# Performance work log

Measured on AMD Instinct MI355X. Metric: run time of the kernel, lower is better.

## Reference

```python
import jax, jax.numpy as jnp
import numpy as np

B, IN, OUT, NVAL = 8192, 4096, 4096, 1024

def setup_inputs() -> dict:
    key = jax.random.key(0)
    k1, k2, k3 = jax.random.split(key, 3)
    x = jax.random.normal(k1, (B, IN), dtype=jnp.float32)
    values = jnp.sort(jax.random.normal(k2, (NVAL,), dtype=jnp.float32))
    bias = jnp.zeros((OUT,), dtype=jnp.float32)
    w_idx = jax.random.randint(k3, (OUT, IN), 0, NVAL, dtype=jnp.int64)
    return {"x": x, "values": values, "bias": bias, "w_idx": w_idx}

def reference(x, values, bias, w_idx):
    # Gather dense weight [OUT, IN] from the codebook, then F.linear: x @ W^T + b
    weight = values[w_idx]
    return jnp.einsum('bi,oi->bo', x, weight) + bias
```

## Files before the change

### kernel.cpp

```cpp
#include <hip/hip_runtime.h>
#include <cstdint>
#include <cstddef>


#define BB 8192
#define KK 4096
#define OO 4096
#define NVALS 1024
#define BM 256
#define BN 256
#define BKT 64

typedef unsigned short u16;
typedef __bf16 bf16x8 __attribute__((ext_vector_type(8)));
typedef float f32x4 __attribute__((ext_vector_type(4)));
typedef unsigned short u16x8 __attribute__((ext_vector_type(8)));
typedef int i32x4 __attribute__((ext_vector_type(4)));

__device__ __forceinline__ u16 f2bf(float f) {
  uint32_t u = __builtin_bit_cast(uint32_t, f);
  u += 0x7FFFu + ((u >> 16) & 1u);
  return (u16)(u >> 16);
}

__global__ void cast_x_kernel(const float* __restrict__ x, u16* __restrict__ xh,
                              int n8) {
  int stride = gridDim.x * blockDim.x;
  for (int i = blockIdx.x * blockDim.x + threadIdx.x; i < n8; i += stride) {
    f32x4 v0 = ((const f32x4*)x)[2 * i];
    f32x4 v1 = ((const f32x4*)x)[2 * i + 1];
    u16x8 h;
#pragma unroll
    for (int j = 0; j < 4; ++j) {
      h[j] = f2bf(v0[j]);
      h[4 + j] = f2bf(v1[j]);
    }
    ((u16x8*)xh)[i] = h;
  }
}

__global__ void dequant_w_kernel(const int* __restrict__ w_idx,
                                 const float* __restrict__ values,
                                 u16* __restrict__ wh, int n8) {
  __shared__ u16 vtab[NVALS];
  for (int i = threadIdx.x; i < NVALS; i += blockDim.x) vtab[i] = f2bf(values[i]);
  __syncthreads();
  int stride = gridDim.x * blockDim.x;
  for (int i = blockIdx.x * blockDim.x + threadIdx.x; i < n8; i += stride) {
    i32x4 a = ((const i32x4*)w_idx)[2 * i];
    i32x4 b = ((const i32x4*)w_idx)[2 * i + 1];
    u16x8 h;
#pragma unroll
    for (int j = 0; j < 4; ++j) {
      h[j] = vtab[a[j] & (NVALS - 1)];
      h[4 + j] = vtab[b[j] & (NVALS - 1)];
    }
    ((u16x8*)wh)[i] = h;
  }
}

__device__ __forceinline__ void stage16(const u16* g, u16* l) {
  __builtin_amdgcn_global_load_lds(
      (const __attribute__((address_space(1))) uint32_t*)g,
      (__attribute__((address_space(3))) uint32_t*)l, 16, 0, 0);
}
__device__ __forceinline__ bf16x8 ldfrag(const u16* p) {
  return __builtin_bit_cast(bf16x8, *(const u16x8*)p);
}
#define BAR()                               \
  do {                                      \
    __asm__ volatile("" ::: "memory");      \
    __builtin_amdgcn_s_barrier();           \
    __asm__ volatile("" ::: "memory");      \
  } while (0)
#define VMCNT6() __asm__ volatile("s_waitcnt vmcnt(6)" ::: "memory")
#define VMCNT0() __asm__ volatile("s_waitcnt vmcnt(0)" ::: "memory")

template <int MH, int NH>
__device__ __forceinline__ void mfma_quad(bf16x8 (&aR)[4][2], bf16x8 (&bR)[4][2],
                                          f32x4 (&acc)[8][4]) {
  __builtin_amdgcn_s_setprio(1);
#pragma unroll
  for (int mq = 0; mq < 4; ++mq)
#pragma unroll
    for (int n2 = 0; n2 < 2; ++n2)
#pragma unroll
      for (int kk = 0; kk < 2; ++kk)
        acc[MH * 4 + mq][NH * 2 + n2] = __builtin_amdgcn_mfma_f32_16x16x32_bf16(
            aR[mq][kk], bR[NH * 2 + n2][kk], acc[MH * 4 + mq][NH * 2 + n2], 0, 0, 0);
  __builtin_amdgcn_s_setprio(0);
}

template <bool ST1, bool ST2, int VM>
__device__ __forceinline__ void ktile(
    u16* CA, u16* CB, u16* OA, const u16* __restrict__ xh,
    const u16* __restrict__ wh, size_t kY, size_t k2, size_t (&srcAX)[2],
    size_t (&srcBX)[2], int (&dstAX)[2], int (&dstBX)[2], int adr, int bdr,
    int chk0, int chk1, bf16x8 (&aR)[4][2], bf16x8 (&bR)[4][2],
    f32x4 (&acc)[8][4]) {
  constexpr size_t srcAY = (size_t)64 * KK;
  constexpr size_t srcBY = (size_t)32 * KK;
  constexpr int dstAY = 64 * BKT;
  constexpr int dstBY = 32 * BKT;
#pragma unroll
  for (int mq = 0; mq < 4; ++mq) {
    aR[mq][0] = ldfrag(CA + adr + chk0 + mq * 1024);
    aR[mq][1] = ldfrag(CA + adr + chk1 + mq * 1024);
  }
#pragma unroll
  for (int n = 0; n < 2; ++n) {
    bR[n][0] = ldfrag(CB + bdr + chk0 + n * 1024);
    bR[n][1] = ldfrag(CB + bdr + chk1 + n * 1024);
  }
  if (ST1) {
#pragma unroll
    for (int i = 0; i < 2; ++i)
      stage16(xh + srcAX[i] + srcAY + kY, OA + dstAX[i] + dstAY);
  }
  BAR();
  mfma_quad<0, 0>(aR, bR, acc);
  BAR();
#pragma unroll
  for (int n = 2; n < 4; ++n) {
    bR[n][0] = ldfrag(CB + bdr + chk0 + n * 1024);
    bR[n][1] = ldfrag(CB + bdr + chk1 + n * 1024);
  }
  if (ST2) {
#pragma unroll
    for (int i = 0; i < 2; ++i) stage16(xh + srcAX[i] + k2, CA + dstAX[i]);
  }
  BAR();
  mfma_quad<0, 1>(aR, bR, acc);
  BAR();
#pragma unroll
  for (int mq = 0; mq < 4; ++mq) {
    aR[mq][0] = ldfrag(CA + adr + chk0 + (4 + mq) * 1024);
    aR[mq][1] = ldfrag(CA + adr + chk1 + (4 + mq) * 1024);
  }
  if (ST2) {
#pragma unroll
    for (int i = 0; i < 2; ++i) stage16(wh + srcBX[i] + k2, CB + dstBX[i]);
  }
  BAR();
  mfma_quad<1, 1>(aR, bR, acc);
  BAR();
  if (ST2) {
#pragma unroll
    for (int i = 0; i < 2; ++i)
      stage16(wh + srcBX[i] + srcBY + k2, CB + dstBX[i] + dstBY);
  }
  BAR();
  mfma_quad<1, 0>(aR, bR, acc);
  if (VM == 0) VMCNT6();
  if (VM == 1) VMCNT0();
  BAR();
}

__global__ __launch_bounds__(512, 2) void gemm8_kernel(
    const u16* __restrict__ xh, const u16* __restrict__ wh,
    const float* __restrict__ bias, float* __restrict__ out) {
  __shared__ __align__(16) u16 lds[4 * BM * BKT];
  u16* const A0 = lds;
  u16* const A1 = lds + BM * BKT;
  u16* const B0 = lds + 2 * BM * BKT;
  u16* const B1 = lds + 3 * BM * BKT;

  int wg = blockIdx.x;
  int cpx = gridDim.x >> 3;
  int swz = (wg & 7) * cpx + (wg >> 3);
  constexpr int NTN = OO / BN;
  int tm = swz / NTN;
  int tn = swz % NTN;

  const int t = threadIdx.x;
  const int lane = t & 63;
  const int wv = t >> 6;
  const int wm = wv >> 2;
  const int wn = wv & 3;

  size_t srcAX[2], srcBX[2];
  int dstAX[2], dstBX[2];
#pragma unroll
  for (int i = 0; i < 2; ++i) {
    int j = i * 512 + t;
    int rl = j >> 3;
    int ch = j & 7;
    int chs = ch ^ (rl & 7);
    int rA = (rl & 63) + ((rl >> 6) << 7);
    int rB = (rl & 31) + ((rl >> 5) << 6);
    srcAX[i] = (size_t)(tm * BM + rA) * KK + chs * 8;
    srcBX[i] = (size_t)(tn * BN + rB) * KK + chs * 8;
    dstAX[i] = rA * BKT + ch * 8;
    dstBX[i] = rB * BKT + ch * 8;
  }
  constexpr size_t srcAY = (size_t)64 * KK;
  constexpr size_t srcBY = (size_t)32 * KK;
  constexpr int dstAY = 64 * BKT;
  constexpr int dstBY = 32 * BKT;

  const int adr = (wm * 128 + (lane & 15)) * BKT;
  const int bdr = (wn * 64 + (lane & 15)) * BKT;
  const int chk0 = (((lane >> 4) ^ (lane & 7))) * 8;
  const int chk1 = ((4 + (lane >> 4)) ^ (lane & 7)) * 8;

  f32x4 acc[8][4];
#pragma unroll
  for (int m = 0; m < 8; ++m)
#pragma unroll
    for (int n = 0; n < 4; ++n) acc[m][n] = f32x4{0.f, 0.f, 0.f, 0.f};
  bf16x8 aR[4][2], bR[4][2];

#pragma unroll
  for (int i = 0; i < 2; ++i) stage16(xh + srcAX[i], A0 + dstAX[i]);
#pragma unroll
  for (int i = 0; i < 2; ++i) stage16(xh + srcAX[i] + srcAY, A0 + dstAX[i] + dstAY);
#pragma unroll
  for (int i = 0; i < 2; ++i) stage16(wh + srcBX[i], B0 + dstBX[i]);
#pragma unroll
  for (int i = 0; i < 2; ++i) stage16(wh + srcBX[i] + srcBY, B0 + dstBX[i] + dstBY);
#pragma unroll
  for (int i = 0; i < 2; ++i) stage16(xh + srcAX[i] + BKT, A1 + dstAX[i]);
#pragma unroll
  for (int i = 0; i < 2; ++i) stage16(wh + srcBX[i] + BKT, B1 + dstBX[i]);
#pragma unroll
  for (int i = 0; i < 2; ++i)
    stage16(wh + srcBX[i] + srcBY + BKT, B1 + dstBX[i] + dstBY);
  VMCNT6();
  BAR();

#pragma unroll 1
  for (int it = 0; it < 31; ++it) {
    size_t s0 = 2 * (size_t)it;
    ktile<true, true, 0>(A0, B0, A1, xh, wh, (s0 + 1) * BKT, (s0 + 2) * BKT,
                         srcAX, srcBX, dstAX, dstBX, adr, bdr, chk0, chk1, aR,
                         bR, acc);
    ktile<true, true, 0>(A1, B1, A0, xh, wh, (s0 + 2) * BKT, (s0 + 3) * BKT,
                         srcAX, srcBX, dstAX, dstBX, adr, bdr, chk0, chk1, aR,
                         bR, acc);
  }
  ktile<true, false, 1>(A0, B0, A1, xh, wh, (size_t)63 * BKT, 0, srcAX, srcBX,
                        dstAX, dstBX, adr, bdr, chk0, chk1, aR, bR, acc);
  ktile<false, false, 2>(A1, B1, A0, xh, wh, 0, 0, srcAX, srcBX, dstAX, dstBX,
                         adr, bdr, chk0, chk1, aR, bR, acc);

#pragma unroll
  for (int n = 0; n < 4; ++n) {
    int col = tn * BN + wn * 64 + n * 16 + (lane & 15);
    float bv = bias[col];
#pragma unroll
    for (int m = 0; m < 8; ++m) {
      int row = tm * BM + wm * 128 + m * 16 + ((lane >> 4) << 2);
#pragma unroll
      for (int r = 0; r < 4; ++r)
        out[(size_t)(row + r) * OO + col] = acc[m][n][r] + bv;
    }
  }
}

__global__ __launch_bounds__(256) void gemm_direct_kernel(
    const float* __restrict__ x, const int* __restrict__ w_idx,
    const float* __restrict__ values, const float* __restrict__ bias,
    float* __restrict__ out) {
  constexpr int K = KK;
  constexpr int NTN = OO / 128;
  __shared__ __align__(16) u16 Ah[128 * 32];
  __shared__ __align__(16) u16 Bh[128 * 32];
  __shared__ u16 vtab[NVALS];
  int wg = blockIdx.x;
  int cpx = gridDim.x >> 3;
  int swz = (wg & 7) * cpx + (wg >> 3);
  int tm = swz / NTN, tn = swz % NTN;
  int t = threadIdx.x, lane = t & 63, wave = t >> 6;
  int wr = wave >> 1, wc = wave & 1;
  for (int i = t; i < NVALS; i += 256) vtab[i] = f2bf(values[i]);
  __syncthreads();
  int r0 = t >> 2, cb = (t & 3) * 8;
  const size_t arow = (size_t)(tm * 128 + r0) * K + cb;
  const size_t brow = (size_t)(tn * 128 + r0) * K + cb;
  const size_t half_off = (size_t)64 * K;
  const int dst = t * 8;
  f32x4 acc[4][4];
#pragma unroll
  for (int m = 0; m < 4; ++m)
#pragma unroll
    for (int n = 0; n < 4; ++n) acc[m][n] = f32x4{0.f, 0.f, 0.f, 0.f};
  const int a_off = (wr * 64 + (lane & 15)) * 32 + (lane >> 4) * 8;
  const int b_off = (wc * 64 + (lane & 15)) * 32 + (lane >> 4) * 8;
  for (int kt = 0; kt < K; kt += 32) {
#pragma unroll
    for (int hh = 0; hh < 2; ++hh) {
      const float* s = x + arow + (size_t)hh * half_off + kt;
      f32x4 v0 = *(const f32x4*)s;
      f32x4 v1 = *(const f32x4*)(s + 4);
      u16x8 hv;
#pragma unroll
      for (int j = 0; j < 4; ++j) {
        hv[j] = f2bf(v0[j]);
        hv[4 + j] = f2bf(v1[j]);
      }
      *(u16x8*)(Ah + dst + hh * 2048) = hv;
    }
#pragma unroll
    for (int hh = 0; hh < 2; ++hh) {
      const int* s = w_idx + brow + (size_t)hh * half_off + kt;
      i32x4 i0v = *(const i32x4*)s;
      i32x4 i1v = *(const i32x4*)(s + 4);
      u16x8 hv;
#pragma unroll
      for (int j = 0; j < 4; ++j) {
        hv[j] = vtab[i0v[j] & (NVALS - 1)];
        hv[4 + j] = vtab[i1v[j] & (NVALS - 1)];
      }
      *(u16x8*)(Bh + dst + hh * 2048) = hv;
    }
    __syncthreads();
    bf16x8 ahf[4], bhf[4];
#pragma unroll
    for (int m = 0; m < 4; ++m) ahf[m] = ldfrag(Ah + a_off + m * 512);
#pragma unroll
    for (int n = 0; n < 4; ++n) bhf[n] = ldfrag(Bh + b_off + n * 512);
#pragma unroll
    for (int m = 0; m < 4; ++m)
#pragma unroll
      for (int n = 0; n < 4; ++n)
        acc[m][n] = __builtin_amdgcn_mfma_f32_16x16x32_bf16(ahf[m], bhf[n],
                                                            acc[m][n], 0, 0, 0);
    __syncthreads();
  }
  float bv[4];
  int coln[4];
#pragma unroll
  for (int n = 0; n < 4; ++n) {
    coln[n] = tn * 128 + wc * 64 + n * 16 + (lane & 15);
    bv[n] = bias[coln[n]];
  }
#pragma unroll
  for (int m = 0; m < 4; ++m) {
    int rowb = tm * 128 + wr * 64 + m * 16 + (lane >> 4) * 4;
#pragma unroll
    for (int n = 0; n < 4; ++n)
#pragma unroll
      for (int r = 0; r < 4; ++r)
        out[(size_t)(rowb + r) * OO + coln[n]] = acc[m][n][r] + bv[n];
  }
}

extern "C" void kernel_launch(void* const* d_in, const int* in_sizes, int n_in,
                              void* d_out, int out_size, void* d_ws, size_t ws_size,
                              hipStream_t stream) {
  const float* x      = (const float*)d_in[0];
  const float* values = (const float*)d_in[1];
  const float* bias   = (const float*)d_in[2];
  const int*   w_idx  = (const int*)d_in[3];
  float* out = (float*)d_out;

  const size_t xN = (size_t)BB * KK;
  const size_t wN = (size_t)OO * KK;
  const size_t need = (xN + wN) * sizeof(u16);

  if (ws_size >= need) {
    u16* xh = (u16*)d_ws;
    u16* wh = xh + xN;
    cast_x_kernel<<<2048, 256, 0, stream>>>(x, xh, (int)(xN / 8));
    dequant_w_kernel<<<2048, 256, 0, stream>>>(w_idx, values, wh, (int)(wN / 8));
    dim3 grid((BB / BM) * (OO / BN));
    gemm8_kernel<<<grid, 512, 0, stream>>>(xh, wh, bias, out);
  } else {
    dim3 grid((BB / 128) * (OO / 128));
    gemm_direct_kernel<<<grid, 256, 0, stream>>>(x, w_idx, values, bias, out);
  }
}
```

Before: 487.0 us.

## Reorder MFMA phases by K-half and rebalance async LDS staging across phases

Splits each k-tile's MFMA work by k-half (KI) across all four N fragments instead of by N-half, so each phase loads only one k-chunk of A and B fragments. The second half of the B tile for the next stage is now issued in the same phase as A's second half, and the current buffers' first halves are refilled together later in the tile. The wait count drops from 6 to 4 outstanding loads. The intent is to spread global-to-LDS traffic more evenly against compute and shorten register live ranges. The risk is that the changed wait counts or buffer-reuse order introduce stalls or LDS hazards.

```diff
diff --git a/kernel.cpp b/kernel.cpp
--- a/kernel.cpp
+++ b/kernel.cpp
@@ -73,28 +73,26 @@
     __builtin_amdgcn_s_barrier();           \
     __asm__ volatile("" ::: "memory");      \
   } while (0)
-#define VMCNT6() __asm__ volatile("s_waitcnt vmcnt(6)" ::: "memory")
+#define VMCNT4() __asm__ volatile("s_waitcnt vmcnt(4)" ::: "memory")
 #define VMCNT0() __asm__ volatile("s_waitcnt vmcnt(0)" ::: "memory")
 
-template <int MH, int NH>
-__device__ __forceinline__ void mfma_quad(bf16x8 (&aR)[4][2], bf16x8 (&bR)[4][2],
-                                          f32x4 (&acc)[8][4]) {
+template <int MH, int KI>
+__device__ __forceinline__ void mfma_set(bf16x8 (&aR)[4][2], bf16x8 (&bR)[4][2],
+                                         f32x4 (&acc)[8][4]) {
   __builtin_amdgcn_s_setprio(1);
 #pragma unroll
   for (int mq = 0; mq < 4; ++mq)
 #pragma unroll
-    for (int n2 = 0; n2 < 2; ++n2)
-#pragma unroll
-      for (int kk = 0; kk < 2; ++kk)
-        acc[MH * 4 + mq][NH * 2 + n2] = __builtin_amdgcn_mfma_f32_16x16x32_bf16(
-            aR[mq][kk], bR[NH * 2 + n2][kk], acc[MH * 4 + mq][NH * 2 + n2], 0, 0, 0);
+    for (int n = 0; n < 4; ++n)
+      acc[MH * 4 + mq][n] = __builtin_amdgcn_mfma_f32_16x16x32_bf16(
+          aR[mq][KI], bR[n][KI], acc[MH * 4 + mq][n], 0, 0, 0);
   __builtin_amdgcn_s_setprio(0);
 }
 
-template <bool ST1, bool ST2, int VM>
+template <bool ST12, bool ST3, int VM>
 __device__ __forceinline__ void ktile(
-    u16* CA, u16* CB, u16* OA, const u16* __restrict__ xh,
-    const u16* __restrict__ wh, size_t kY, size_t k2, size_t (&srcAX)[2],
+    u16* CA, u16* CB, u16* OA, u16* OB, const u16* __restrict__ xh,
+    const u16* __restrict__ wh, size_t kn, size_t k2, size_t (&srcAX)[2],
     size_t (&srcBX)[2], int (&dstAX)[2], int (&dstBX)[2], int adr, int bdr,
     int chk0, int chk1, bf16x8 (&aR)[4][2], bf16x8 (&bR)[4][2],
     f32x4 (&acc)[8][4]) {
@@ -103,55 +101,47 @@
   constexpr int dstAY = 64 * BKT;
   constexpr int dstBY = 32 * BKT;
 #pragma unroll
-  for (int mq = 0; mq < 4; ++mq) {
-    aR[mq][0] = ldfrag(CA + adr + chk0 + mq * 1024);
-    aR[mq][1] = ldfrag(CA + adr + chk1 + mq * 1024);
-  }
-#pragma unroll
-  for (int n = 0; n < 2; ++n) {
-    bR[n][0] = ldfrag(CB + bdr + chk0 + n * 1024);
-    bR[n][1] = ldfrag(CB + bdr + chk1 + n * 1024);
-  }
-  if (ST1) {
+  for (int mq = 0; mq < 4; ++mq) aR[mq][0] = ldfrag(CA + adr + chk0 + mq * 1024);
+#pragma unroll
+  for (int n = 0; n < 4; ++n) bR[n][0] = ldfrag(CB + bdr + chk0 + n * 1024);
+  if (ST12) {
 #pragma unroll
     for (int i = 0; i < 2; ++i)
-      stage16(xh + srcAX[i] + srcAY + kY, OA + dstAX[i] + dstAY);
-  }
-  BAR();
-  mfma_quad<0, 0>(aR, bR, acc);
-  BAR();
-#pragma unroll
-  for (int n = 2; n < 4; ++n) {
-    bR[n][0] = ldfrag(CB + bdr + chk0 + n * 1024);
-    bR[n][1] = ldfrag(CB + bdr + chk1 + n * 1024);
-  }
-  if (ST2) {
+      stage16(xh + srcAX[i] + srcAY + kn, OA + dstAX[i] + dstAY);
+  }
+  BAR();
+  mfma_set<0, 0>(aR, bR, acc);
+  BAR();
+#pragma unroll
+  for (int mq = 0; mq < 4; ++mq) aR[mq][1] = ldfrag(CA + adr + chk1 + mq * 1024);
+#pragma unroll
+  for (int n = 0; n < 4; ++n) bR[n][1] = ldfrag(CB + bdr + chk1 + n * 1024);
+  if (ST12) {
+#pragma unroll
+    for (int i = 0; i < 2; ++i)
+      stage16(wh + srcBX[i] + srcBY + kn, OB + dstBX[i] + dstBY);
+  }
+  BAR();
+  mfma_set<0, 1>(aR, bR, acc);
+  BAR();
+#pragma unroll
+  for (int mq = 0; mq < 4; ++mq)
+    aR[mq][0] = ldfrag(CA + adr + chk0 + (4 + mq) * 1024);
+  if (ST3) {
 #pragma unroll
     for (int i = 0; i < 2; ++i) stage16(xh + srcAX[i] + k2, CA + dstAX[i]);
-  }
-  BAR();
-  mfma_quad<0, 1>(aR, bR, acc);
-  BAR();
-#pragma unroll
-  for (int mq = 0; mq < 4; ++mq) {
-    aR[mq][0] = ldfrag(CA + adr + chk0 + (4 + mq) * 1024);
+#pragma unroll
+    for (int i = 0; i < 2; ++i) stage16(wh + srcBX[i] + k2, CB + dstBX[i]);
+  }
+  BAR();
+  mfma_set<1, 0>(aR, bR, acc);
+  BAR();
+#pragma unroll
+  for (int mq = 0; mq < 4; ++mq)
     aR[mq][1] = ldfrag(CA + adr + chk1 + (4 + mq) * 1024);
-  }
-  if (ST2) {
-#pragma unroll
-    for (int i = 0; i < 2; ++i) stage16(wh + srcBX[i] + k2, CB + dstBX[i]);
-  }
-  BAR();
-  mfma_quad<1, 1>(aR, bR, acc);
-  BAR();
-  if (ST2) {
-#pragma unroll
-    for (int i = 0; i < 2; ++i)
-      stage16(wh + srcBX[i] + srcBY + k2, CB + dstBX[i] + dstBY);
-  }
-  BAR();
-  mfma_quad<1, 0>(aR, bR, acc);
-  if (VM == 0) VMCNT6();
+  BAR();
+  mfma_set<1, 1>(aR, bR, acc);
+  if (VM == 0) VMCNT4();
   if (VM == 1) VMCNT0();
   BAR();
 }
@@ -222,26 +212,23 @@
   for (int i = 0; i < 2; ++i) stage16(xh + srcAX[i] + BKT, A1 + dstAX[i]);
 #pragma unroll
   for (int i = 0; i < 2; ++i) stage16(wh + srcBX[i] + BKT, B1 + dstBX[i]);
-#pragma unroll
-  for (int i = 0; i < 2; ++i)
-    stage16(wh + srcBX[i] + srcBY + BKT, B1 + dstBX[i] + dstBY);
-  VMCNT6();
+  VMCNT4();
   BAR();
 
 #pragma unroll 1
   for (int it = 0; it < 31; ++it) {
     size_t s0 = 2 * (size_t)it;
-    ktile<true, true, 0>(A0, B0, A1, xh, wh, (s0 + 1) * BKT, (s0 + 2) * BKT,
+    ktile<true, true, 0>(A0, B0, A1, B1, xh, wh, (s0 + 1) * BKT, (s0 + 2) * BKT,
                          srcAX, srcBX, dstAX, dstBX, adr, bdr, chk0, chk1, aR,
                          bR, acc);
-    ktile<true, true, 0>(A1, B1, A0, xh, wh, (s0 + 2) * BKT, (s0 + 3) * BKT,
+    ktile<true, true, 0>(A1, B1, A0, B0, xh, wh, (s0 + 2) * BKT, (s0 + 3) * BKT,
                          srcAX, srcBX, dstAX, dstBX, adr, bdr, chk0, chk1, aR,
                          bR, acc);
   }
-  ktile<true, false, 1>(A0, B0, A1, xh, wh, (size_t)63 * BKT, 0, srcAX, srcBX,
-                        dstAX, dstBX, adr, bdr, chk0, chk1, aR, bR, acc);
-  ktile<false, false, 2>(A1, B1, A0, xh, wh, 0, 0, srcAX, srcBX, dstAX, dstBX,
-                         adr, bdr, chk0, chk1, aR, bR, acc);
+  ktile<true, false, 1>(A0, B0, A1, B1, xh, wh, (size_t)63 * BKT, 0, srcAX,
+                        srcBX, dstAX, dstBX, adr, bdr, chk0, chk1, aR, bR, acc);
+  ktile<false, false, 2>(A1, B1, A0, B0, xh, wh, 0, 0, srcAX, srcBX, dstAX,
+                         dstBX, adr, bdr, chk0, chk1, aR, bR, acc);
 
 #pragma unroll
   for (int n = 0; n < 4; ++n) {
```

After: 495.3 us. About the same (+1.7%).
